# Kernel tuning notes

Measured on AMD Instinct MI355X. Metric: run time of the kernel, lower is better.

## Reference

```python
import jax, jax.numpy as jnp
import numpy as np

NUM_USERS = 100000
NUM_ITEMS = 50000
HIDDEN = 64
NUM_LAYERS = 3
NUM_EDGES = 1200000
N = NUM_USERS + NUM_ITEMS


def setup_inputs() -> dict:
    key = jax.random.key(0)
    k_e, k_u, k_i, k_w, k_b = jax.random.split(key, 5)
    edge_index = jax.random.randint(k_e, (2, NUM_EDGES), 0, N, dtype=jnp.int32)
    users_emb = jax.random.normal(k_u, (NUM_USERS, HIDDEN), dtype=jnp.float32) * 0.01
    items_emb = jax.random.normal(k_i, (NUM_ITEMS, HIDDEN), dtype=jnp.float32) * 0.01
    # GCNConv linear weights (glorot-ish) and zero biases, stacked over layers
    scale = 1.0 / np.sqrt(HIDDEN)
    Ws = jax.random.uniform(k_w, (NUM_LAYERS, HIDDEN, HIDDEN), dtype=jnp.float32,
                            minval=-scale, maxval=scale)
    bs = jnp.zeros((NUM_LAYERS, HIDDEN), dtype=jnp.float32)
    return {"edge_index": edge_index, "users_emb": users_emb,
            "items_emb": items_emb, "Ws": Ws, "bs": bs}


def reference(edge_index, users_emb, items_emb, Ws, bs):
    # GraphSAGEModel.forward: concat user/item embeddings, run num_layers GCNConv
    # (PyG defaults: add self-loops, symmetric D^-1/2 A D^-1/2 normalization, bias).
    x = jnp.concatenate([users_emb, items_emb], axis=0)  # [N, H]

    self_loops = jnp.arange(N, dtype=edge_index.dtype)
    src = jnp.concatenate([edge_index[0], self_loops])  # [E+N]
    dst = jnp.concatenate([edge_index[1], self_loops])

    ones = jnp.ones(src.shape[0], dtype=x.dtype)
    deg = jax.ops.segment_sum(ones, dst, num_segments=N)  # in-degree incl self loop
    dinv = jnp.where(deg > 0, jax.lax.rsqrt(deg), 0.0)
    norm = dinv[src] * dinv[dst]  # [E+N], graph-constant across layers

    for l in range(NUM_LAYERS):
        h = x @ Ws[l]                       # linear transform [N, H]
        msg = h[src] * norm[:, None]        # gather + scale
        x = jax.ops.segment_sum(msg, dst, num_segments=N) + bs[l]
    return (x[:NUM_USERS], users_emb, x[NUM_USERS:], items_emb)
```

## Files before the change

kernel.cpp:

```cpp
#include <hip/hip_runtime.h>
#include <hip/hip_fp16.h>
#include <type_traits>

#define NU 100000
#define NI 50000
#define NN 150000
#define HH 64
#define NE 1200000

#define SCAN_CHUNK 1024
#define NBLK ((NN + SCAN_CHUNK - 1) / SCAN_CHUNK)

__global__ void k_concat(const float4* __restrict__ users, const float4* __restrict__ items,
                         const float* __restrict__ dinv,
                         __half2* __restrict__ xs, float4* __restrict__ out) {
    int i = blockIdx.x * blockDim.x + threadIdx.x;
    const int TOT = NN * (HH / 4);
    const int UB  = NU * (HH / 4);
    if (i >= TOT) return;
    float4 v;
    if (i < UB) {
        v = users[i];
        out[UB + i] = v;
    } else {
        int j = i - UB;
        v = items[j];
        out[2 * UB + NI * (HH / 4) + j] = v;
    }
    float dv = dinv[i >> 4];
    xs[2 * i]     = __halves2half2(__float2half_rn(v.x * dv), __float2half_rn(v.y * dv));
    xs[2 * i + 1] = __halves2half2(__float2half_rn(v.z * dv), __float2half_rn(v.w * dv));
}

__global__ void k_rank(const int4* __restrict__ dst4, int* __restrict__ counts,
                       int4* __restrict__ rank4) {
    int t = blockIdx.x * blockDim.x + threadIdx.x;
    if (t >= NE / 4) return;
    int4 d = dst4[t];
    int4 r;
    r.x = atomicAdd(&counts[d.x], 1);
    r.y = atomicAdd(&counts[d.y], 1);
    r.z = atomicAdd(&counts[d.z], 1);
    r.w = atomicAdd(&counts[d.w], 1);
    rank4[t] = r;
}

__global__ void k_scan_reduce(const int* __restrict__ counts, int* __restrict__ bsum,
                              float* __restrict__ dinv) {
    __shared__ int sd[256];
    int t = threadIdx.x;
    int base = blockIdx.x * SCAN_CHUNK + t * 4;
    int s = 0;
    if (base + 3 < NN) {
        int4 v = *(const int4*)(counts + base);
        s = v.x + v.y + v.z + v.w;
        dinv[base + 0] = rsqrtf((float)(v.x + 1));
        dinv[base + 1] = rsqrtf((float)(v.y + 1));
        dinv[base + 2] = rsqrtf((float)(v.z + 1));
        dinv[base + 3] = rsqrtf((float)(v.w + 1));
    } else {
        for (int i = 0; i < 4; ++i)
            if (base + i < NN) {
                int c = counts[base + i];
                s += c;
                dinv[base + i] = rsqrtf((float)(c + 1));
            }
    }
    sd[t] = s; __syncthreads();
    for (int off = 128; off > 0; off >>= 1) {
        if (t < off) sd[t] += sd[t + off];
        __syncthreads();
    }
    if (t == 0) bsum[blockIdx.x] = sd[0];
}

__global__ void k_scan_top(int* __restrict__ bsum, int* __restrict__ row_ptr) {
    __shared__ int sd[256];
    int t = threadIdx.x;
    int v = (t < NBLK) ? bsum[t] : 0;
    sd[t] = v; __syncthreads();
    for (int off = 1; off < 256; off <<= 1) {
        int x = (t >= off) ? sd[t - off] : 0;
        __syncthreads();
        sd[t] += x;
        __syncthreads();
    }
    if (t < NBLK) bsum[t] = sd[t] - v;
    if (t == 0) row_ptr[NN] = NE;
}

__global__ void k_scan_chunks(const int* __restrict__ counts, const int* __restrict__ boff,
                              int* __restrict__ row_ptr) {
    __shared__ int sd[256];
    int t = threadIdx.x;
    int base = blockIdx.x * SCAN_CHUNK + t * 4;
    int c[4];
#pragma unroll
    for (int i = 0; i < 4; ++i) c[i] = (base + i < NN) ? counts[base + i] : 0;
    int tt = c[0] + c[1] + c[2] + c[3];
    sd[t] = tt; __syncthreads();
    for (int off = 1; off < 256; off <<= 1) {
        int x = (t >= off) ? sd[t - off] : 0;
        __syncthreads();
        sd[t] += x;
        __syncthreads();
    }
    int off0 = boff[blockIdx.x] + (sd[t] - tt);
    int run = 0;
#pragma unroll
    for (int i = 0; i < 4; ++i) {
        if (base + i < NN) row_ptr[base + i] = off0 + run;
        run += c[i];
    }
}

__global__ void k_fill(const int4* __restrict__ src4, const int4* __restrict__ dst4,
                       const int4* __restrict__ rank4, const int* __restrict__ row_ptr,
                       int* __restrict__ col) {
    int t = blockIdx.x * blockDim.x + threadIdx.x;
    if (t >= NE / 8) return;
    int4 s0 = src4[2 * t],  s1 = src4[2 * t + 1];
    int4 d0 = dst4[2 * t],  d1 = dst4[2 * t + 1];
    int4 r0 = rank4[2 * t], r1 = rank4[2 * t + 1];
    int p0 = row_ptr[d0.x], p1 = row_ptr[d0.y], p2 = row_ptr[d0.z], p3 = row_ptr[d0.w];
    int p4 = row_ptr[d1.x], p5 = row_ptr[d1.y], p6 = row_ptr[d1.z], p7 = row_ptr[d1.w];
    col[p0 + r0.x] = s0.x;
    col[p1 + r0.y] = s0.y;
    col[p2 + r0.z] = s0.z;
    col[p3 + r0.w] = s0.w;
    col[p4 + r1.x] = s1.x;
    col[p5 + r1.y] = s1.y;
    col[p6 + r1.z] = s1.z;
    col[p7 + r1.w] = s1.w;
}

#define G1(c) __half2float(x[(size_t)(c) * HH + lane])
__global__ __launch_bounds__(256) void k_aggregate(const __half* __restrict__ x,
                                                   __half* __restrict__ y,
                                                   const float* __restrict__ dinv,
                                                   const int* __restrict__ row_ptr,
                                                   const int* __restrict__ col) {
    int lane = threadIdx.x & 63;
    int wave = blockIdx.x * 4 + (threadIdx.x >> 6);
    int na = wave * 2;
    if (na >= NN) return;
    int nb = na + 1;

    float acca = G1(na);
    float accb = G1(nb);
    int ea = row_ptr[na], enda = row_ptr[na + 1];
    int eb = enda,        endb = row_ptr[nb + 1];

    while (ea + 4 <= enda && eb + 4 <= endb) {
        int a0 = col[ea], a1 = col[ea + 1], a2 = col[ea + 2], a3 = col[ea + 3];
        int b0 = col[eb], b1 = col[eb + 1], b2 = col[eb + 2], b3 = col[eb + 3];
        float va0 = G1(a0), va1 = G1(a1), va2 = G1(a2), va3 = G1(a3);
        float vb0 = G1(b0), vb1 = G1(b1), vb2 = G1(b2), vb3 = G1(b3);
        acca += (va0 + va1) + (va2 + va3);
        accb += (vb0 + vb1) + (vb2 + vb3);
        ea += 4; eb += 4;
    }
    for (; ea + 4 <= enda; ea += 4) {
        int c0 = col[ea], c1 = col[ea + 1], c2 = col[ea + 2], c3 = col[ea + 3];
        acca += (G1(c0) + G1(c1)) + (G1(c2) + G1(c3));
    }
    if (ea + 2 <= enda) {
        int c0 = col[ea], c1 = col[ea + 1];
        acca += G1(c0) + G1(c1);
        ea += 2;
    }
    if (ea < enda) acca += G1(col[ea]);
    for (; eb + 4 <= endb; eb += 4) {
        int c0 = col[eb], c1 = col[eb + 1], c2 = col[eb + 2], c3 = col[eb + 3];
        accb += (G1(c0) + G1(c1)) + (G1(c2) + G1(c3));
    }
    if (eb + 2 <= endb) {
        int c0 = col[eb], c1 = col[eb + 1];
        accb += G1(c0) + G1(c1);
        eb += 2;
    }
    if (eb < endb) accb += G1(col[eb]);

    y[(size_t)na * HH + lane] = __float2half_rn(dinv[na] * acca);
    y[(size_t)nb * HH + lane] = __float2half_rn(dinv[nb] * accb);
}
#undef G1

#define GR 128
#define XSS 65
template <typename OutT>
__global__ __launch_bounds__(256) void k_gemm(const __half* __restrict__ y,
                                              const float* __restrict__ W,
                                              const float* __restrict__ b,
                                              const float* __restrict__ dinv,
                                              OutT* __restrict__ out_lo,
                                              OutT* __restrict__ out_hi,
                                              int split) {
    __shared__ float xs[GR * XSS];
    __shared__ float ws[HH * HH];
    int t = threadIdx.x;
    int rowBase = blockIdx.x * GR;

    {
        const float4* W4 = (const float4*)W;
        float4* ws4 = (float4*)ws;
#pragma unroll
        for (int i = 0; i < 4; ++i) ws4[i * 256 + t] = W4[i * 256 + t];
    }
#pragma unroll
    for (int it = 0; it < 4; ++it) {
        int g = it * 256 + t;
        int r = g >> 3;
        int c0 = (g & 7) * 8;
        int row = rowBase + r;
        if (row < NN) {
            int4 raw = *(const int4*)(y + (size_t)row * HH + c0);
            __half2 h0 = *(__half2*)&raw.x, h1 = *(__half2*)&raw.y;
            __half2 h2 = *(__half2*)&raw.z, h3 = *(__half2*)&raw.w;
            float2 f0 = __half22float2(h0), f1 = __half22float2(h1);
            float2 f2 = __half22float2(h2), f3 = __half22float2(h3);
            float* dp = xs + r * XSS + c0;
            dp[0] = f0.x; dp[1] = f0.y; dp[2] = f1.x; dp[3] = f1.y;
            dp[4] = f2.x; dp[5] = f2.y; dp[6] = f3.x; dp[7] = f3.y;
        }
    }
    __syncthreads();

    int tx = t & 7;
    int ty = t >> 3;
    int j0 = tx * 8;
    int r0 = ty * 4;

    float acc[4][8];
#pragma unroll
    for (int i = 0; i < 4; ++i)
#pragma unroll
        for (int j = 0; j < 8; ++j) acc[i][j] = 0.f;

    for (int k = 0; k < HH; ++k) {
        float4 w0 = *(const float4*)(ws + k * HH + j0);
        float4 w1 = *(const float4*)(ws + k * HH + j0 + 4);
        float wv[8] = {w0.x, w0.y, w0.z, w0.w, w1.x, w1.y, w1.z, w1.w};
#pragma unroll
        for (int i = 0; i < 4; ++i) {
            float xv = xs[(r0 + i) * XSS + k];
#pragma unroll
            for (int j = 0; j < 8; ++j) acc[i][j] += xv * wv[j];
        }
    }

    float bj[8];
#pragma unroll
    for (int j = 0; j < 8; ++j) bj[j] = b[j0 + j];

#pragma unroll
    for (int i = 0; i < 4; ++i) {
        int r = rowBase + r0 + i;
        if (r >= NN) continue;
        if constexpr (std::is_same_v<OutT, float>) {
            float4 o0 = make_float4(acc[i][0] + bj[0], acc[i][1] + bj[1],
                                    acc[i][2] + bj[2], acc[i][3] + bj[3]);
            float4 o1 = make_float4(acc[i][4] + bj[4], acc[i][5] + bj[5],
                                    acc[i][6] + bj[6], acc[i][7] + bj[7]);
            float* d = (r < split) ? ((float*)out_lo + (size_t)r * HH)
                                   : ((float*)out_hi + (size_t)(r - split) * HH);
            *(float4*)(d + j0) = o0;
            *(float4*)(d + j0 + 4) = o1;
        } else {
            float dv = dinv[r];
            __half2 h[4];
#pragma unroll
            for (int j = 0; j < 4; ++j)
                h[j] = __halves2half2(
                    __float2half_rn((acc[i][2 * j]     + bj[2 * j])     * dv),
                    __float2half_rn((acc[i][2 * j + 1] + bj[2 * j + 1]) * dv));
            __half* d = (__half*)out_lo + (size_t)r * HH + j0;
            *(int4*)d = *(int4*)h;
        }
    }
}

extern "C" void kernel_launch(void* const* d_in, const int* in_sizes, int n_in,
                              void* d_out, int out_size, void* d_ws, size_t ws_size,
                              hipStream_t stream) {
    const int*   edge  = (const int*)d_in[0];
    const int*   src   = edge;
    const int*   dst   = edge + NE;
    const float* users = (const float*)d_in[1];
    const float* items = (const float*)d_in[2];
    const float* Ws    = (const float*)d_in[3];
    const float* bs    = (const float*)d_in[4];
    float*       out   = (float*)d_out;

    char* w = (char*)d_ws;
    __half* Xs0     = (__half*)w; w += (size_t)NN * HH * 2;
    __half* Xs1     = (__half*)w; w += (size_t)NN * HH * 2;
    float*  dinv    = (float*)w;  w += (size_t)NN * 4;
    int*    counts  = (int*)w;    w += (size_t)NN * 4;
    int*    row_ptr = (int*)w;    w += (size_t)(NN + 1) * 4;
    w += 4;
    int*    bsum    = (int*)w;    w += 256 * 4;
    int*    col     = (int*)w;    w += (size_t)NE * 4;
    int*    rank    = (int*)w;    w += (size_t)NE * 4;
    (void)ws_size; (void)in_sizes; (void)n_in; (void)out_size;

    hipMemsetAsync(counts, 0, (size_t)NN * sizeof(int), stream);

    k_rank<<<(NE / 4 + 255) / 256, 256, 0, stream>>>((const int4*)dst, counts, (int4*)rank);
    k_scan_reduce<<<NBLK, 256, 0, stream>>>(counts, bsum, dinv);
    k_concat<<<(NN * (HH / 4) + 255) / 256, 256, 0, stream>>>(
        (const float4*)users, (const float4*)items, dinv, (__half2*)Xs0, (float4*)out);
    k_scan_top<<<1, 256, 0, stream>>>(bsum, row_ptr);
    k_scan_chunks<<<NBLK, 256, 0, stream>>>(counts, bsum, row_ptr);
    k_fill<<<(NE / 8 + 255) / 256, 256, 0, stream>>>(
        (const int4*)src, (const int4*)dst, (const int4*)rank, row_ptr, col);

    const int AGG_BLOCKS  = NN / 8;
    const int GEMM_BLOCKS = (NN + GR - 1) / GR;

    k_aggregate<<<AGG_BLOCKS, 256, 0, stream>>>(Xs0, Xs1, dinv, row_ptr, col);
    k_gemm<__half><<<GEMM_BLOCKS, 256, 0, stream>>>(
        Xs1, Ws + 0 * HH * HH, bs + 0 * HH, dinv, Xs0, Xs0, NN);
    k_aggregate<<<AGG_BLOCKS, 256, 0, stream>>>(Xs0, Xs1, dinv, row_ptr, col);
    k_gemm<__half><<<GEMM_BLOCKS, 256, 0, stream>>>(
        Xs1, Ws + 1 * HH * HH, bs + 1 * HH, dinv, Xs0, Xs0, NN);
    k_aggregate<<<AGG_BLOCKS, 256, 0, stream>>>(Xs0, Xs1, dinv, row_ptr, col);
    k_gemm<float><<<GEMM_BLOCKS, 256, 0, stream>>>(
        Xs1, Ws + 2 * HH * HH, bs + 2 * HH, dinv,
        out , out + (size_t)2 * NU * HH , NU);
}
```

Baseline: 415.1 us.

## Gather four neighbor rows per wave with 8-byte loads and shuffle reduction

Restructures the aggregation kernel so each wave splits into four 16-lane groups. Each group loads a different neighbor row with 8-byte vector loads (4 halves per lane), and the partial sums are combined with cross-lane xor shuffles. Out-of-range edges point at an appended zero padding row, which removes the tail loops in favor of uniform masked iterations. The goal is more memory-level parallelism and fewer, wider gather instructions. The cost is extra shuffles, two small memsets, and wasted loads on padded slots for low-degree nodes.

```diff
diff --git a/kernel.cpp b/kernel.cpp
--- a/kernel.cpp
+++ b/kernel.cpp
@@ -134,7 +134,6 @@
     col[p7 + r1.w] = s1.w;
 }
 
-#define G1(c) __half2float(x[(size_t)(c) * HH + lane])
 __global__ __launch_bounds__(256) void k_aggregate(const __half* __restrict__ x,
                                                    __half* __restrict__ y,
                                                    const float* __restrict__ dinv,
@@ -145,46 +144,71 @@
     int na = wave * 2;
     if (na >= NN) return;
     int nb = na + 1;
-
-    float acca = G1(na);
-    float accb = G1(nb);
+    int q  = lane >> 4;
+    int f4 = (lane & 15) << 2;
+
+    float a0 = 0.f, a1 = 0.f, a2 = 0.f, a3 = 0.f;
+    float b0 = 0.f, b1 = 0.f, b2 = 0.f, b3 = 0.f;
+
+#define GATHER(r, c0, c1, c2, c3)                                          \
+    {                                                                      \
+        uint2 raw = *(const uint2*)(x + (size_t)(r) * HH + f4);            \
+        float2 f0 = __half22float2(*(__half2*)&raw.x);                     \
+        float2 f1 = __half22float2(*(__half2*)&raw.y);                     \
+        c0 += f0.x; c1 += f0.y; c2 += f1.x; c3 += f1.y;                    \
+    }
+
     int ea = row_ptr[na], enda = row_ptr[na + 1];
     int eb = enda,        endb = row_ptr[nb + 1];
 
-    while (ea + 4 <= enda && eb + 4 <= endb) {
-        int a0 = col[ea], a1 = col[ea + 1], a2 = col[ea + 2], a3 = col[ea + 3];
-        int b0 = col[eb], b1 = col[eb + 1], b2 = col[eb + 2], b3 = col[eb + 3];
-        float va0 = G1(a0), va1 = G1(a1), va2 = G1(a2), va3 = G1(a3);
-        float vb0 = G1(b0), vb1 = G1(b1), vb2 = G1(b2), vb3 = G1(b3);
-        acca += (va0 + va1) + (va2 + va3);
-        accb += (vb0 + vb1) + (vb2 + vb3);
-        ea += 4; eb += 4;
-    }
-    for (; ea + 4 <= enda; ea += 4) {
-        int c0 = col[ea], c1 = col[ea + 1], c2 = col[ea + 2], c3 = col[ea + 3];
-        acca += (G1(c0) + G1(c1)) + (G1(c2) + G1(c3));
-    }
-    if (ea + 2 <= enda) {
-        int c0 = col[ea], c1 = col[ea + 1];
-        acca += G1(c0) + G1(c1);
-        ea += 2;
-    }
-    if (ea < enda) acca += G1(col[ea]);
-    for (; eb + 4 <= endb; eb += 4) {
-        int c0 = col[eb], c1 = col[eb + 1], c2 = col[eb + 2], c3 = col[eb + 3];
-        accb += (G1(c0) + G1(c1)) + (G1(c2) + G1(c3));
-    }
-    if (eb + 2 <= endb) {
-        int c0 = col[eb], c1 = col[eb + 1];
-        accb += G1(c0) + G1(c1);
-        eb += 2;
-    }
-    if (eb < endb) accb += G1(col[eb]);
-
-    y[(size_t)na * HH + lane] = __float2half_rn(dinv[na] * acca);
-    y[(size_t)nb * HH + lane] = __float2half_rn(dinv[nb] * accb);
-}
-#undef G1
+    {
+        int ia = ea + q - 1;
+        int ib = eb + q - 1;
+        int rA = (q == 0) ? na : ((ia < enda) ? col[ia] : NN);
+        int rB = (q == 0) ? nb : ((ib < endb) ? col[ib] : NN);
+        GATHER(rA, a0, a1, a2, a3);
+        GATHER(rB, b0, b1, b2, b3);
+        ea += 3; eb += 3;
+    }
+    while (ea < enda || eb < endb) {
+        int iA1 = ea + q,     iA2 = ea + 4 + q;
+        int iB1 = eb + q,     iB2 = eb + 4 + q;
+        int rA1 = (iA1 < enda) ? col[iA1] : NN;
+        int rA2 = (iA2 < enda) ? col[iA2] : NN;
+        int rB1 = (iB1 < endb) ? col[iB1] : NN;
+        int rB2 = (iB2 < endb) ? col[iB2] : NN;
+        GATHER(rA1, a0, a1, a2, a3);
+        GATHER(rA2, a0, a1, a2, a3);
+        GATHER(rB1, b0, b1, b2, b3);
+        GATHER(rB2, b0, b1, b2, b3);
+        ea += 8; eb += 8;
+    }
+#undef GATHER
+
+    a0 += __shfl_xor(a0, 16); a1 += __shfl_xor(a1, 16);
+    a2 += __shfl_xor(a2, 16); a3 += __shfl_xor(a3, 16);
+    b0 += __shfl_xor(b0, 16); b1 += __shfl_xor(b1, 16);
+    b2 += __shfl_xor(b2, 16); b3 += __shfl_xor(b3, 16);
+    a0 += __shfl_xor(a0, 32); a1 += __shfl_xor(a1, 32);
+    a2 += __shfl_xor(a2, 32); a3 += __shfl_xor(a3, 32);
+    b0 += __shfl_xor(b0, 32); b1 += __shfl_xor(b1, 32);
+    b2 += __shfl_xor(b2, 32); b3 += __shfl_xor(b3, 32);
+
+    if (lane < 32) {
+        int   n  = (q == 0) ? na : nb;
+        float dv = dinv[n];
+        float s0 = (q == 0) ? a0 : b0;
+        float s1 = (q == 0) ? a1 : b1;
+        float s2 = (q == 0) ? a2 : b2;
+        float s3 = (q == 0) ? a3 : b3;
+        __half2 h0 = __halves2half2(__float2half_rn(dv * s0), __float2half_rn(dv * s1));
+        __half2 h1 = __halves2half2(__float2half_rn(dv * s2), __float2half_rn(dv * s3));
+        uint2 packed;
+        packed.x = *(unsigned int*)&h0;
+        packed.y = *(unsigned int*)&h1;
+        *(uint2*)(y + (size_t)n * HH + f4) = packed;
+    }
+}
 
 #define GR 128
 #define XSS 65
@@ -293,8 +317,8 @@
     float*       out   = (float*)d_out;
 
     char* w = (char*)d_ws;
-    __half* Xs0     = (__half*)w; w += (size_t)NN * HH * 2;
-    __half* Xs1     = (__half*)w; w += (size_t)NN * HH * 2;
+    __half* Xs0     = (__half*)w; w += (size_t)(NN + 1) * HH * 2;
+    __half* Xs1     = (__half*)w; w += (size_t)(NN + 1) * HH * 2;
     float*  dinv    = (float*)w;  w += (size_t)NN * 4;
     int*    counts  = (int*)w;    w += (size_t)NN * 4;
     int*    row_ptr = (int*)w;    w += (size_t)(NN + 1) * 4;
@@ -305,6 +329,8 @@
     (void)ws_size; (void)in_sizes; (void)n_in; (void)out_size;
 
     hipMemsetAsync(counts, 0, (size_t)NN * sizeof(int), stream);
+    hipMemsetAsync(Xs0 + (size_t)NN * HH, 0, HH * sizeof(__half), stream);
+    hipMemsetAsync(Xs1 + (size_t)NN * HH, 0, HH * sizeof(__half), stream);
 
     k_rank<<<(NE / 4 + 255) / 256, 256, 0, stream>>>((const int4*)dst, counts, (int4*)rank);
     k_scan_reduce<<<NBLK, 256, 0, stream>>>(counts, bsum, dinv);
```

Result: no change. 414.6 us (-0.1%).
